# Kernel tuning notes

Measured on AMD Instinct MI355X. Metric: run time of the kernel, lower is better.

## Reference

```python
import jax, jax.numpy as jnp
import numpy as np

IN_DIM = 256   # opt.word_vec_size
MEM_DIM = 256  # opt.rnn_size // num_directions
N_LEAVES = 131072  # 2**17, complete binary tree


def setup_inputs() -> dict:
    key = jax.random.key(0)
    ks = jax.random.split(key, 8)
    s = 0.05  # weight scale
    return {
        # leaf word2vec embeddings, in-order leaf sequence of the tree
        "x": jax.random.normal(ks[0], (N_LEAVES, IN_DIM), jnp.float32),
        # BinaryTreeLeafModule params (Linear as x @ W + b)
        "Wcx": jax.random.normal(ks[1], (IN_DIM, MEM_DIM), jnp.float32) * s,
        "bcx": jnp.zeros((MEM_DIM,), jnp.float32),
        "Wox": jax.random.normal(ks[2], (IN_DIM, MEM_DIM), jnp.float32) * s,
        "box": jnp.zeros((MEM_DIM,), jnp.float32),
        # BinaryTreeComposer params: 4 left-child gates (i, lf, rf, u) fused
        # along the output dim, likewise 4 right-child gates.
        "Wl": jax.random.normal(ks[3], (MEM_DIM, 4 * MEM_DIM), jnp.float32) * s,
        "bl": jnp.zeros((4 * MEM_DIM,), jnp.float32),
        "Wr": jax.random.normal(ks[4], (MEM_DIM, 4 * MEM_DIM), jnp.float32) * s,
        "br": jnp.zeros((4 * MEM_DIM,), jnp.float32),
        "lengths": N_LEAVES,  # max sequence length for output padding
    }


def reference(x, Wcx, bcx, Wox, box, Wl, bl, Wr, br, lengths):
    m = Wcx.shape[1]
    # ---- BinaryTreeLeafModule, batched over all leaves ----
    c = x @ Wcx + bcx                                   # [n, m]
    h = jax.nn.sigmoid(x @ Wox + box) * jnp.tanh(c)     # [n, m]
    leaf_h = h  # in-order cat of leaf outputs == recursive cat([lo, ro])

    # ---- BinaryTreeComposer, one batched step per tree level ----
    # Loop over log2(n_leaves) levels of a complete binary tree; each
    # iteration composes adjacent sibling pairs (shapes static -> jit-safe).
    while c.shape[0] > 1:
        lc, rc = c[0::2], c[1::2]
        lh, rh = h[0::2], h[1::2]
        g = (lh @ Wl + bl) + (rh @ Wr + br)             # [n/2, 4m]
        gi, glf, grf, gu = jnp.split(g, 4, axis=-1)
        i = jax.nn.sigmoid(gi)
        lf = jax.nn.sigmoid(glf)
        rf = jax.nn.sigmoid(grf)
        u = jnp.tanh(gu)
        c = i * u + lf * lc + rf * rc                   # [n/2, m]
        h = jnp.tanh(c)                                 # gate_output=False

    # ---- root post-processing (as in original when tree.parent is None) ----
    output = leaf_h[:, None, :]                         # [n_leaves, 1, m]
    supl = int(lengths) - output.shape[0]
    if supl > 0:
        output = jnp.concatenate(
            [output, jnp.zeros((supl, 1, m), output.dtype)], axis=0)
    c_root = c[:, None, :]                              # [1, 1, m]
    h_root = h[:, None, :]                              # [1, 1, m]
    return output, (c_root, h_root)
```

## Files before the change

kernel.cpp:

```cpp
#include <hip/hip_runtime.h>
#include <cstdint>
#include <cstddef>


typedef float floatx4 __attribute__((ext_vector_type(4)));
typedef __bf16 bf16x8 __attribute__((ext_vector_type(8)));

typedef __attribute__((address_space(1))) unsigned int u32g;
typedef __attribute__((address_space(3))) unsigned int u32l;

__device__ __forceinline__ void async_copy16(const void* g, void* l) {
  __builtin_amdgcn_global_load_lds((u32g*)(uintptr_t)g, (u32l*)l, 16, 0, 0);
}

__device__ __forceinline__ float sigf(float x) {
  return __frcp_rn(1.f + __expf(-x));
}
__device__ __forceinline__ float tanh_f(float x) {
  float e = __expf(-2.f * x);
  return __builtin_fmaf(2.f, __frcp_rn(1.f + e), -1.f);
}

__global__ void prep_leaf(const float* __restrict__ Wcx, const float* __restrict__ bcx,
                          const float* __restrict__ Wox, const float* __restrict__ box,
                          __bf16* __restrict__ WleafT, float* __restrict__ bleaf) {
  int n = blockIdx.x;
  int k = threadIdx.x;
  const float* src = (n < 256) ? Wcx : Wox;
  int col = n & 255;
  WleafT[n * 256 + k] = (__bf16)src[k * 256 + col];
  if (k == 0) bleaf[n] = (n < 256) ? bcx[col] : box[col];
}

__global__ void prep_cat(const float* __restrict__ Wl, const float* __restrict__ bl,
                         const float* __restrict__ Wr, const float* __restrict__ br,
                         __bf16* __restrict__ WcatT, float* __restrict__ bcat) {
  int n = blockIdx.x;
  for (int k = threadIdx.x; k < 512; k += 256) {
    const float* src = (k < 256) ? Wl : Wr;
    WcatT[n * 512 + k] = (__bf16)src[(size_t)(k & 255) * 1024 + n];
  }
  if (threadIdx.x == 0) bcat[n] = bl[n] + br[n];
}

__global__ __launch_bounds__(256, 4) void leaf_kernel(
    const float* __restrict__ x,
    const __bf16* __restrict__ WT,
    const float* __restrict__ bleaf,
    __bf16* __restrict__ c_out,
    __bf16* __restrict__ h_out,
    float* __restrict__ h_out32)
{
  __shared__ __bf16 SMEM[16384];
  const int tid  = threadIdx.x;
  const int wave = tid >> 6;
  const int lane = tid & 63;
  const int quad = lane >> 4;
  const int l15  = lane & 15;

  const int lid = blockIdx.y * gridDim.x + blockIdx.x;
  const int nwg = gridDim.x * gridDim.y;
  const int swz = (lid & 7) * (nwg >> 3) + (lid >> 3);
  const int j0  = (swz & 3) * 64;
  const int bm  = swz >> 2;

  floatx4 acc[2][8];
#pragma unroll
  for (int r = 0; r < 2; ++r)
#pragma unroll
    for (int f = 0; f < 8; ++f) acc[r][f] = (floatx4){0.f, 0.f, 0.f, 0.f};

  for (int kk = 0; kk < 256; kk += 64) {
#pragma unroll
    for (int it = 0; it < 4; ++it) {
      int f = it * 256 + tid;
      int row = f >> 3, cc = f & 7;
      int cb = cc ^ (row & 7);
      const float4* gx = (const float4*)(x + (size_t)(bm * 128 + row) * 256 + kk + cc * 8);
      float4 u = gx[0], v = gx[1];
      bf16x8 a8 = {(__bf16)u.x, (__bf16)u.y, (__bf16)u.z, (__bf16)u.w,
                   (__bf16)v.x, (__bf16)v.y, (__bf16)v.z, (__bf16)v.w};
      *(bf16x8*)&SMEM[row * 64 + cb * 8] = a8;
      int ng = ((row >> 6) << 8) + j0 + (row & 63);
      async_copy16(WT + (size_t)ng * 256 + kk + cb * 8, &SMEM[8192 + (f & ~63) * 8]);
    }
    __syncthreads();
#pragma unroll
    for (int s = 0; s < 2; ++s) {
      const int b  = (s * 4 + quad) ^ (l15 & 7);
      const int kb = b * 8;
      bf16x8 a0 = *(const bf16x8*)&SMEM[(wave * 32 + l15) * 64 + kb];
      bf16x8 a1 = *(const bf16x8*)&SMEM[(wave * 32 + 16 + l15) * 64 + kb];
#pragma unroll
      for (int f = 0; f < 8; ++f) {
        bf16x8 b8 = *(const bf16x8*)&SMEM[8192 + (f * 16 + l15) * 64 + kb];
        acc[0][f] = __builtin_amdgcn_mfma_f32_16x16x32_bf16(a0, b8, acc[0][f], 0, 0, 0);
        acc[1][f] = __builtin_amdgcn_mfma_f32_16x16x32_bf16(a1, b8, acc[1][f], 0, 0, 0);
      }
    }
    __syncthreads();
  }

  const int R0 = bm * 128;
#pragma unroll
  for (int r = 0; r < 2; ++r) {
#pragma unroll
    for (int q = 0; q < 4; ++q) {
      int col = j0 + q * 16 + l15;
      float bC = bleaf[col];
      float bO = bleaf[256 + col];
#pragma unroll
      for (int reg = 0; reg < 4; ++reg) {
        int lr = wave * 32 + r * 16 + quad * 4 + reg;
        int lc = q * 16 + l15;
        float c = acc[r][q][reg] + bC;
        float o = acc[r][q + 4][reg] + bO;
        float h = sigf(o) * tanh_f(c);
        h_out32[(size_t)(R0 + lr) * 256 + col] = h;
        int ch  = (lc >> 3) ^ ((lr ^ (lr >> 3)) & 7);
        int idx = lr * 64 + ch * 8 + (lc & 7);
        SMEM[idx]        = (__bf16)c;
        SMEM[8192 + idx] = (__bf16)h;
      }
    }
  }
  __syncthreads();
#pragma unroll
  for (int i = 0; i < 4; ++i) {
    int unit = i * 256 + tid;
    int lr = unit >> 3, k = unit & 7;
    int ch = k ^ ((lr ^ (lr >> 3)) & 7);
    bf16x8 vc = *(const bf16x8*)&SMEM[lr * 64 + ch * 8];
    bf16x8 vh = *(const bf16x8*)&SMEM[8192 + lr * 64 + ch * 8];
    size_t g = (size_t)(R0 + lr) * 256 + j0 + k * 8;
    *(bf16x8*)&c_out[g] = vc;
    *(bf16x8*)&h_out[g] = vh;
  }
}

template <typename OUT>
__global__ __launch_bounds__(256, 4) void tree_level(
    const __bf16* __restrict__ h_in,
    const __bf16* __restrict__ c_in,
    const __bf16* __restrict__ WT,
    const float* __restrict__ bcat,
    OUT* __restrict__ c_out,
    OUT* __restrict__ h_out,
    const int M)
{
  __shared__ __bf16 SMEM[16384];
  const int tid  = threadIdx.x;
  const int wave = tid >> 6;
  const int lane = tid & 63;
  const int quad = lane >> 4;
  const int l15  = lane & 15;

  const int lid = blockIdx.y * gridDim.x + blockIdx.x;
  const int nwg = gridDim.x * gridDim.y;
  const int swz = (lid & 7) * (nwg >> 3) + (lid >> 3);
  const int j0  = (swz & 7) * 32;
  const int bm  = swz >> 3;

  floatx4 acc[2][8];
#pragma unroll
  for (int r = 0; r < 2; ++r)
#pragma unroll
    for (int f = 0; f < 8; ++f) acc[r][f] = (floatx4){0.f, 0.f, 0.f, 0.f};

  for (int kk = 0; kk < 512; kk += 64) {
#pragma unroll
    for (int it = 0; it < 4; ++it) {
      int f = it * 256 + tid;
      int row = f >> 3, cc = f & 7;
      int cb = cc ^ (row & 7);
      int rg = bm * 128 + row;
      rg = rg < M ? rg : M - 1;
      async_copy16(h_in + (size_t)rg * 512 + kk + cb * 8, &SMEM[(f & ~63) * 8]);
      int ng = ((row >> 5) << 8) + j0 + (row & 31);
      async_copy16(WT + (size_t)ng * 512 + kk + cb * 8, &SMEM[8192 + (f & ~63) * 8]);
    }
    __syncthreads();
#pragma unroll
    for (int s = 0; s < 2; ++s) {
      const int b  = (s * 4 + quad) ^ (l15 & 7);
      const int kb = b * 8;
      bf16x8 a0 = *(const bf16x8*)&SMEM[(wave * 32 + l15) * 64 + kb];
      bf16x8 a1 = *(const bf16x8*)&SMEM[(wave * 32 + 16 + l15) * 64 + kb];
#pragma unroll
      for (int f = 0; f < 8; ++f) {
        bf16x8 b8 = *(const bf16x8*)&SMEM[8192 + (f * 16 + l15) * 64 + kb];
        acc[0][f] = __builtin_amdgcn_mfma_f32_16x16x32_bf16(a0, b8, acc[0][f], 0, 0, 0);
        acc[1][f] = __builtin_amdgcn_mfma_f32_16x16x32_bf16(a1, b8, acc[1][f], 0, 0, 0);
      }
    }
    __syncthreads();
  }

  {
    const int maxr = 2 * M - 1;
#pragma unroll
    for (int i = 0; i < 4; ++i) {
      int chunk = i * 256 + tid;
      int row = chunk >> 2, piece = chunk & 3;
      int gr = bm * 256 + row;
      gr = gr < maxr ? gr : maxr;
      async_copy16(c_in + (size_t)gr * 256 + j0 + piece * 8,
                   &SMEM[8192 + (chunk & ~63) * 8]);
    }
  }
  __syncthreads();

  if constexpr (sizeof(OUT) == 2) {
#pragma unroll
    for (int r = 0; r < 2; ++r) {
#pragma unroll
      for (int q = 0; q < 2; ++q) {
        int col = j0 + q * 16 + l15;
        float bi  = bcat[col];
        float blf = bcat[256 + col];
        float brf = bcat[512 + col];
        float bu  = bcat[768 + col];
#pragma unroll
        for (int reg = 0; reg < 4; ++reg) {
          int lr  = wave * 32 + r * 16 + quad * 4 + reg;
          int lcc = q * 16 + l15;
          int row = bm * 128 + lr;
          float cn = 0.f, hn = 0.f;
          if (row < M) {
            float lc = (float)SMEM[8192 + (2 * lr) * 32 + lcc];
            float rc = (float)SMEM[8192 + (2 * lr + 1) * 32 + lcc];
            float iv = sigf(acc[r][0 + q][reg] + bi);
            float lf = sigf(acc[r][2 + q][reg] + blf);
            float rf = sigf(acc[r][4 + q][reg] + brf);
            float uv = tanh_f(acc[r][6 + q][reg] + bu);
            cn = iv * uv + lf * lc + rf * rc;
            hn = tanh_f(cn);
          }
          int ch  = (lcc >> 3) ^ ((lr ^ (lr >> 2)) & 3);
          int idx = lr * 32 + ch * 8 + (lcc & 7);
          SMEM[idx]        = (__bf16)cn;
          SMEM[4096 + idx] = (__bf16)hn;
        }
      }
    }
    __syncthreads();
#pragma unroll
    for (int i = 0; i < 2; ++i) {
      int unit = i * 256 + tid;
      int lr = unit >> 2, k = unit & 3;
      int gr = bm * 128 + lr;
      if (gr < M) {
        int ch = k ^ ((lr ^ (lr >> 2)) & 3);
        bf16x8 vc = *(const bf16x8*)&SMEM[lr * 32 + ch * 8];
        bf16x8 vh = *(const bf16x8*)&SMEM[4096 + lr * 32 + ch * 8];
        size_t g = (size_t)gr * 256 + j0 + k * 8;
        *(bf16x8*)((__bf16*)c_out + g) = vc;
        *(bf16x8*)((__bf16*)h_out + g) = vh;
      }
    }
  } else {
#pragma unroll
    for (int r = 0; r < 2; ++r) {
#pragma unroll
      for (int q = 0; q < 2; ++q) {
        int col = j0 + q * 16 + l15;
        float bi  = bcat[col];
        float blf = bcat[256 + col];
        float brf = bcat[512 + col];
        float bu  = bcat[768 + col];
#pragma unroll
        for (int reg = 0; reg < 4; ++reg) {
          int lr  = wave * 32 + r * 16 + quad * 4 + reg;
          int lcc = q * 16 + l15;
          int row = bm * 128 + lr;
          if (row < M) {
            float lc = (float)SMEM[8192 + (2 * lr) * 32 + lcc];
            float rc = (float)SMEM[8192 + (2 * lr + 1) * 32 + lcc];
            float iv = sigf(acc[r][0 + q][reg] + bi);
            float lf = sigf(acc[r][2 + q][reg] + blf);
            float rf = sigf(acc[r][4 + q][reg] + brf);
            float uv = tanh_f(acc[r][6 + q][reg] + bu);
            float cn = iv * uv + lf * lc + rf * rc;
            float hn = tanh_f(cn);
            size_t idx = (size_t)row * 256 + col;
            c_out[idx] = (OUT)cn;
            h_out[idx] = (OUT)hn;
          }
        }
      }
    }
  }
}

extern "C" void kernel_launch(void* const* d_in, const int* in_sizes, int n_in,
                              void* d_out, int out_size, void* d_ws, size_t ws_size,
                              hipStream_t stream) {
  const float* x   = (const float*)d_in[0];
  const float* Wcx = (const float*)d_in[1];
  const float* bcx = (const float*)d_in[2];
  const float* Wox = (const float*)d_in[3];
  const float* box = (const float*)d_in[4];
  const float* Wl  = (const float*)d_in[5];
  const float* bl  = (const float*)d_in[6];
  const float* Wr  = (const float*)d_in[7];
  const float* br  = (const float*)d_in[8];

  const size_t LEAF = (size_t)131072 * 256;
  const size_t MiB  = 1ull << 20;
  char* ws = (char*)d_ws;

  __bf16* WleafT = (__bf16*)(ws);
  __bf16* WcatT  = (__bf16*)(ws + 262144);
  float*  bleaf  = (float*)(ws + 262144 + 1048576);
  float*  bcat   = bleaf + 512;

  int slog = 17;
  size_t ra_sz = 0, rb_sz = 0;
  while (slog > 11) {
    size_t SL  = (size_t)1 << slog;
    size_t nsl = (size_t)(131072 >> slog);
    ra_sz = SL * 512 > nsl * 524288 ? SL * 512 : nsl * 524288;
    rb_sz = SL * 256 > nsl * 262144 ? SL * 256 : nsl * 262144;
    size_t need = 2 * MiB + SL * 1024 + ra_sz + rb_sz + nsl * MiB;
    if (need <= ws_size) break;
    --slog;
  }
  const int SLAB  = 1 << slog;
  const int nslab = 131072 >> slog;

  char*   dyn = ws + 2 * MiB;
  __bf16* LC  = (__bf16*)dyn;
  __bf16* LH  = LC + (size_t)SLAB * 256;
  char*   RA  = (char*)(LH + (size_t)SLAB * 256);
  char*   RB  = RA + ra_sz;
  __bf16* CC  = (__bf16*)(RB + rb_sz);
  __bf16* CH  = CC + (size_t)nslab * 1024 * 256;

  float* out    = (float*)d_out;
  float* leaf_h = out;
  float* c_root = out + LEAF;
  float* h_root = out + LEAF + 256;

  prep_leaf<<<dim3(512), dim3(256), 0, stream>>>(Wcx, bcx, Wox, box, WleafT, bleaf);
  prep_cat<<<dim3(1024), dim3(256), 0, stream>>>(Wl, bl, Wr, br, WcatT, bcat);

  if (nslab == 1) {
    leaf_kernel<<<dim3(4, SLAB / 128), dim3(256), 0, stream>>>(
        x, WleafT, bleaf, LC, LH, leaf_h);

    const __bf16* hin = LH;
    const __bf16* cin = LC;
    for (int lvl = 1; lvl <= slog; ++lvl) {
      const int M = SLAB >> lvl;
      dim3 grid(8, (M + 127) / 128);
      if (lvl == slog) {
        tree_level<float><<<grid, dim3(256), 0, stream>>>(
            hin, cin, WcatT, bcat, c_root, h_root, M);
      } else {
        __bf16* cdst = (__bf16*)((lvl & 1) ? RA : RB);
        __bf16* hdst = cdst + (size_t)M * 256;
        tree_level<__bf16><<<grid, dim3(256), 0, stream>>>(
            hin, cin, WcatT, bcat, cdst, hdst, M);
        hin = hdst; cin = cdst;
      }
    }
  } else {
    const int STOP = slog - 10;
    for (int sl = 0; sl < nslab; ++sl) {
      const size_t R0 = (size_t)sl * SLAB;
      leaf_kernel<<<dim3(4, SLAB / 128), dim3(256), 0, stream>>>(
          x + R0 * 256, WleafT, bleaf, LC, LH, leaf_h + R0 * 256);

      const __bf16* hin = LH;
      const __bf16* cin = LC;
      for (int lvl = 1; lvl <= STOP; ++lvl) {
        const int M = SLAB >> lvl;
        dim3 grid(8, (M + 127) / 128);
        __bf16 *cdst, *hdst;
        if (lvl == STOP) {
          cdst = CC + (size_t)sl * 1024 * 256;
          hdst = CH + (size_t)sl * 1024 * 256;
        } else {
          cdst = (__bf16*)((lvl & 1) ? RA : RB);
          hdst = cdst + (size_t)M * 256;
        }
        tree_level<__bf16><<<grid, dim3(256), 0, stream>>>(
            hin, cin, WcatT, bcat, cdst, hdst, M);
        hin = hdst; cin = cdst;
      }
    }
    {
      const __bf16* hin = CH;
      const __bf16* cin = CC;
      int pp = 1;
      for (int M = (nslab << 10) >> 1; M >= 1; M >>= 1, pp ^= 1) {
        dim3 grid(8, (M + 127) / 128);
        if (M == 1) {
          tree_level<float><<<grid, dim3(256), 0, stream>>>(
              hin, cin, WcatT, bcat, c_root, h_root, 1);
        } else {
          __bf16* cdst = (__bf16*)(pp ? RA : RB);
          __bf16* hdst = cdst + (size_t)M * 256;
          tree_level<__bf16><<<grid, dim3(256), 0, stream>>>(
              hin, cin, WcatT, bcat, cdst, hdst, M);
          hin = hdst; cin = cdst;
        }
      }
    }
  }
}
```

Measured before the change: 711.5 us.

## Double-buffer LDS tiles in leaf and tree GEMM kernels, use fast rcp

Both GEMM kernels now use two LDS buffers so the next K-tile's global loads (async LDS loads for weights and h, register prefetch for x) are issued before the MFMAs on the current tile run. This halves the synchronisation count and hides load latency. LDS per block doubles to 64 KB and launch bounds drop from 4 to 2 blocks per CU, trading occupancy for overlap. Sigmoid and tanh also switch from __frcp_rn to the hardware approximate reciprocal, which is slightly less accurate.

```diff
diff --git a/kernel.cpp b/kernel.cpp
--- a/kernel.cpp
+++ b/kernel.cpp
@@ -14,11 +14,11 @@
 }
 
 __device__ __forceinline__ float sigf(float x) {
-  return __frcp_rn(1.f + __expf(-x));
+  return __builtin_amdgcn_rcpf(1.f + __expf(-x));
 }
 __device__ __forceinline__ float tanh_f(float x) {
   float e = __expf(-2.f * x);
-  return __builtin_fmaf(2.f, __frcp_rn(1.f + e), -1.f);
+  return __builtin_fmaf(2.f, __builtin_amdgcn_rcpf(1.f + e), -1.f);
 }
 
 __global__ void prep_leaf(const float* __restrict__ Wcx, const float* __restrict__ bcx,
@@ -43,7 +43,7 @@
   if (threadIdx.x == 0) bcat[n] = bl[n] + br[n];
 }
 
-__global__ __launch_bounds__(256, 4) void leaf_kernel(
+__global__ __launch_bounds__(256, 2) void leaf_kernel(
     const float* __restrict__ x,
     const __bf16* __restrict__ WT,
     const float* __restrict__ bleaf,
@@ -51,7 +51,7 @@
     __bf16* __restrict__ h_out,
     float* __restrict__ h_out32)
 {
-  __shared__ __bf16 SMEM[16384];
+  __shared__ __bf16 SMEM[32768];
   const int tid  = threadIdx.x;
   const int wave = tid >> 6;
   const int lane = tid & 63;
@@ -70,32 +70,70 @@
 #pragma unroll
     for (int f = 0; f < 8; ++f) acc[r][f] = (floatx4){0.f, 0.f, 0.f, 0.f};
 
-  for (int kk = 0; kk < 256; kk += 64) {
-#pragma unroll
-    for (int it = 0; it < 4; ++it) {
-      int f = it * 256 + tid;
-      int row = f >> 3, cc = f & 7;
-      int cb = cc ^ (row & 7);
-      const float4* gx = (const float4*)(x + (size_t)(bm * 128 + row) * 256 + kk + cc * 8);
-      float4 u = gx[0], v = gx[1];
-      bf16x8 a8 = {(__bf16)u.x, (__bf16)u.y, (__bf16)u.z, (__bf16)u.w,
-                   (__bf16)v.x, (__bf16)v.y, (__bf16)v.z, (__bf16)v.w};
-      *(bf16x8*)&SMEM[row * 64 + cb * 8] = a8;
-      int ng = ((row >> 6) << 8) + j0 + (row & 63);
-      async_copy16(WT + (size_t)ng * 256 + kk + cb * 8, &SMEM[8192 + (f & ~63) * 8]);
-    }
-    __syncthreads();
+  float4 pa[4][2];
+
+#pragma unroll
+  for (int it = 0; it < 4; ++it) {
+    int f = it * 256 + tid;
+    int row = f >> 3, cc = f & 7;
+    int cb = cc ^ (row & 7);
+    const float4* gx = (const float4*)(x + (size_t)(bm * 128 + row) * 256 + cc * 8);
+    pa[it][0] = gx[0]; pa[it][1] = gx[1];
+    int ng = ((row >> 6) << 8) + j0 + (row & 63);
+    async_copy16(WT + (size_t)ng * 256 + cb * 8, &SMEM[8192 + (f & ~63) * 8]);
+  }
+#pragma unroll
+  for (int it = 0; it < 4; ++it) {
+    int f = it * 256 + tid;
+    int row = f >> 3, cc = f & 7;
+    int cb = cc ^ (row & 7);
+    float4 u = pa[it][0], v = pa[it][1];
+    bf16x8 a8 = {(__bf16)u.x, (__bf16)u.y, (__bf16)u.z, (__bf16)u.w,
+                 (__bf16)v.x, (__bf16)v.y, (__bf16)v.z, (__bf16)v.w};
+    *(bf16x8*)&SMEM[row * 64 + cb * 8] = a8;
+  }
+  __syncthreads();
+
+#pragma unroll
+  for (int t = 0; t < 4; ++t) {
+    const int cur = (t & 1) * 16384;
+    const int nxt = 16384 - cur;
+    if (t < 3) {
+      const int kk = (t + 1) * 64;
+#pragma unroll
+      for (int it = 0; it < 4; ++it) {
+        int f = it * 256 + tid;
+        int row = f >> 3, cc = f & 7;
+        int cb = cc ^ (row & 7);
+        const float4* gx = (const float4*)(x + (size_t)(bm * 128 + row) * 256 + kk + cc * 8);
+        pa[it][0] = gx[0]; pa[it][1] = gx[1];
+        int ng = ((row >> 6) << 8) + j0 + (row & 63);
+        async_copy16(WT + (size_t)ng * 256 + kk + cb * 8, &SMEM[nxt + 8192 + (f & ~63) * 8]);
+      }
+    }
 #pragma unroll
     for (int s = 0; s < 2; ++s) {
       const int b  = (s * 4 + quad) ^ (l15 & 7);
       const int kb = b * 8;
-      bf16x8 a0 = *(const bf16x8*)&SMEM[(wave * 32 + l15) * 64 + kb];
-      bf16x8 a1 = *(const bf16x8*)&SMEM[(wave * 32 + 16 + l15) * 64 + kb];
+      bf16x8 a0 = *(const bf16x8*)&SMEM[cur + (wave * 32 + l15) * 64 + kb];
+      bf16x8 a1 = *(const bf16x8*)&SMEM[cur + (wave * 32 + 16 + l15) * 64 + kb];
 #pragma unroll
       for (int f = 0; f < 8; ++f) {
-        bf16x8 b8 = *(const bf16x8*)&SMEM[8192 + (f * 16 + l15) * 64 + kb];
+        bf16x8 b8 = *(const bf16x8*)&SMEM[cur + 8192 + (f * 16 + l15) * 64 + kb];
         acc[0][f] = __builtin_amdgcn_mfma_f32_16x16x32_bf16(a0, b8, acc[0][f], 0, 0, 0);
         acc[1][f] = __builtin_amdgcn_mfma_f32_16x16x32_bf16(a1, b8, acc[1][f], 0, 0, 0);
+      }
+    }
+    if (t < 3) {
+#pragma unroll
+      for (int it = 0; it < 4; ++it) {
+        int f = it * 256 + tid;
+        int row = f >> 3, cc = f & 7;
+        int cb = cc ^ (row & 7);
+        float4 u = pa[it][0], v = pa[it][1];
+        bf16x8 a8 = {(__bf16)u.x, (__bf16)u.y, (__bf16)u.z, (__bf16)u.w,
+                     (__bf16)v.x, (__bf16)v.y, (__bf16)v.z, (__bf16)v.w};
+        *(bf16x8*)&SMEM[nxt + row * 64 + cb * 8] = a8;
       }
     }
     __syncthreads();
@@ -139,7 +177,7 @@
 }
 
 template <typename OUT>
-__global__ __launch_bounds__(256, 4) void tree_level(
+__global__ __launch_bounds__(256, 2) void tree_level(
     const __bf16* __restrict__ h_in,
     const __bf16* __restrict__ c_in,
     const __bf16* __restrict__ WT,
@@ -148,7 +186,7 @@
     OUT* __restrict__ h_out,
     const int M)
 {
-  __shared__ __bf16 SMEM[16384];
+  __shared__ __bf16 SMEM[32768];
   const int tid  = threadIdx.x;
   const int wave = tid >> 6;
   const int lane = tid & 63;
@@ -167,28 +205,46 @@
 #pragma unroll
     for (int f = 0; f < 8; ++f) acc[r][f] = (floatx4){0.f, 0.f, 0.f, 0.f};
 
-  for (int kk = 0; kk < 512; kk += 64) {
-#pragma unroll
-    for (int it = 0; it < 4; ++it) {
-      int f = it * 256 + tid;
-      int row = f >> 3, cc = f & 7;
-      int cb = cc ^ (row & 7);
-      int rg = bm * 128 + row;
-      rg = rg < M ? rg : M - 1;
-      async_copy16(h_in + (size_t)rg * 512 + kk + cb * 8, &SMEM[(f & ~63) * 8]);
-      int ng = ((row >> 5) << 8) + j0 + (row & 31);
-      async_copy16(WT + (size_t)ng * 512 + kk + cb * 8, &SMEM[8192 + (f & ~63) * 8]);
-    }
-    __syncthreads();
+#pragma unroll
+  for (int it = 0; it < 4; ++it) {
+    int f = it * 256 + tid;
+    int row = f >> 3, cc = f & 7;
+    int cb = cc ^ (row & 7);
+    int rg = bm * 128 + row;
+    rg = rg < M ? rg : M - 1;
+    async_copy16(h_in + (size_t)rg * 512 + cb * 8, &SMEM[(f & ~63) * 8]);
+    int ng = ((row >> 5) << 8) + j0 + (row & 31);
+    async_copy16(WT + (size_t)ng * 512 + cb * 8, &SMEM[8192 + (f & ~63) * 8]);
+  }
+  __syncthreads();
+
+#pragma unroll
+  for (int t = 0; t < 8; ++t) {
+    const int cur = (t & 1) * 16384;
+    const int nxt = 16384 - cur;
+    if (t < 7) {
+      const int kk = (t + 1) * 64;
+#pragma unroll
+      for (int it = 0; it < 4; ++it) {
+        int f = it * 256 + tid;
+        int row = f >> 3, cc = f & 7;
+        int cb = cc ^ (row & 7);
+        int rg = bm * 128 + row;
+        rg = rg < M ? rg : M - 1;
+        async_copy16(h_in + (size_t)rg * 512 + kk + cb * 8, &SMEM[nxt + (f & ~63) * 8]);
+        int ng = ((row >> 5) << 8) + j0 + (row & 31);
+        async_copy16(WT + (size_t)ng * 512 + kk + cb * 8, &SMEM[nxt + 8192 + (f & ~63) * 8]);
+      }
+    }
 #pragma unroll
     for (int s = 0; s < 2; ++s) {
       const int b  = (s * 4 + quad) ^ (l15 & 7);
       const int kb = b * 8;
-      bf16x8 a0 = *(const bf16x8*)&SMEM[(wave * 32 + l15) * 64 + kb];
-      bf16x8 a1 = *(const bf16x8*)&SMEM[(wave * 32 + 16 + l15) * 64 + kb];
+      bf16x8 a0 = *(const bf16x8*)&SMEM[cur + (wave * 32 + l15) * 64 + kb];
+      bf16x8 a1 = *(const bf16x8*)&SMEM[cur + (wave * 32 + 16 + l15) * 64 + kb];
 #pragma unroll
       for (int f = 0; f < 8; ++f) {
-        bf16x8 b8 = *(const bf16x8*)&SMEM[8192 + (f * 16 + l15) * 64 + kb];
+        bf16x8 b8 = *(const bf16x8*)&SMEM[cur + 8192 + (f * 16 + l15) * 64 + kb];
         acc[0][f] = __builtin_amdgcn_mfma_f32_16x16x32_bf16(a0, b8, acc[0][f], 0, 0, 0);
         acc[1][f] = __builtin_amdgcn_mfma_f32_16x16x32_bf16(a1, b8, acc[1][f], 0, 0, 0);
       }
@@ -205,7 +261,7 @@
       int gr = bm * 256 + row;
       gr = gr < maxr ? gr : maxr;
       async_copy16(c_in + (size_t)gr * 256 + j0 + piece * 8,
-                   &SMEM[8192 + (chunk & ~63) * 8]);
+                   &SMEM[16384 + (chunk & ~63) * 8]);
     }
   }
   __syncthreads();
@@ -227,8 +283,8 @@
           int row = bm * 128 + lr;
           float cn = 0.f, hn = 0.f;
           if (row < M) {
-            float lc = (float)SMEM[8192 + (2 * lr) * 32 + lcc];
-            float rc = (float)SMEM[8192 + (2 * lr + 1) * 32 + lcc];
+            float lc = (float)SMEM[16384 + (2 * lr) * 32 + lcc];
+            float rc = (float)SMEM[16384 + (2 * lr + 1) * 32 + lcc];
             float iv = sigf(acc[r][0 + q][reg] + bi);
             float lf = sigf(acc[r][2 + q][reg] + blf);
             float rf = sigf(acc[r][4 + q][reg] + brf);
@@ -274,8 +330,8 @@
           int lcc = q * 16 + l15;
           int row = bm * 128 + lr;
           if (row < M) {
-            float lc = (float)SMEM[8192 + (2 * lr) * 32 + lcc];
-            float rc = (float)SMEM[8192 + (2 * lr + 1) * 32 + lcc];
+            float lc = (float)SMEM[16384 + (2 * lr) * 32 + lcc];
+            float rc = (float)SMEM[16384 + (2 * lr + 1) * 32 + lcc];
             float iv = sigf(acc[r][0 + q][reg] + bi);
             float lf = sigf(acc[r][2 + q][reg] + blf);
             float rf = sigf(acc[r][4 + q][reg] + brf);
```

Result: faster. 643.8 us (-9.5%).
